# Kernel tuning notes

Measured on AMD Instinct MI355X. Metric: run time of the kernel, lower is better.

## Reference

```python
import jax, jax.numpy as jnp
import numpy as np

B, N, DIN, DOUT = 8, 2048, 256, 256

def setup_inputs() -> dict:
    key = jax.random.key(0)
    k1, k2, k3 = jax.random.split(key, 3)
    H = jax.random.normal(k1, (B, N, DIN), dtype=jnp.float32)
    G = jax.random.uniform(k2, (B, N, N), dtype=jnp.float32)  # positive -> nonzero row/col sums
    # xavier_uniform-style scale for the weight
    limit = float(np.sqrt(6.0 / (DIN + DOUT)))
    W = jax.random.uniform(k3, (DIN, DOUT), dtype=jnp.float32, minval=-limit, maxval=limit)
    return {"H": H, "G": G, "W": W}

def reference(H, G, W):
    # N_e = H @ W : [b,n,dout]
    N_e = H @ W
    # symmetric part
    G_F = (G + jnp.swapaxes(G, 1, 2)) * 0.5
    # loop over k of outer products == two normalized Gram matrices:
    # G_Sin[i,j] = sum_k G[k,i]*G[k,j] / rowsum_k  == G^T diag(1/rowsum) G
    # G_So[i,j]  = sum_k G[i,k]*G[j,k] / colsum_k  == G diag(1/colsum) G^T
    rs = G.sum(axis=-1)  # [b,n] row sums
    cs = G.sum(axis=-2)  # [b,n] col sums
    G_Sin = jnp.einsum('bki,bkj->bij', G / rs[:, :, None], G)
    G_So = jnp.einsum('bik,bjk->bij', G / cs[:, None, :], G)
    H_out = jnp.concatenate([
        jax.nn.relu(G_F @ N_e),
        jax.nn.relu(G_Sin @ N_e),
        jax.nn.relu(G_So @ N_e),
    ], axis=-1)  # [b,n,3*dout]
    return H_out
```

## Files before the change

kernel.cpp:

```cpp
#include <hip/hip_runtime.h>
#include <hip/hip_bf16.h>


constexpr int NN = 2048;
constexpr long GSTR = (long)NN * NN;
constexpr long SDN = 256L * 2048;

using frag8   = __attribute__((ext_vector_type(8))) short;
using floatx4 = __attribute__((ext_vector_type(4))) float;
using ush8    = __attribute__((ext_vector_type(8))) unsigned short;

__device__ inline unsigned short f2bf(float x) {
    unsigned u = __float_as_uint(x);
    u += 0x7FFF + ((u >> 16) & 1);
    return (unsigned short)(u >> 16);
}
__device__ inline float bf2f(unsigned short h) {
    return __uint_as_float((unsigned)h << 16);
}
__device__ inline ushort2 pk2(float a, float b) {
    union { __hip_bfloat162 h; ushort2 u; } cv;
    cv.h = __float22bfloat162_rn(float2{a, b});
    return cv.u;
}
__device__ inline void gload_lds16(const void* g, void* l) {
    __builtin_amdgcn_global_load_lds(
        (const __attribute__((address_space(1))) void*)g,
        (__attribute__((address_space(3))) void*)l, 16, 0, 0);
}

template <int PHASE>
__global__ __launch_bounds__(256) void gemmF(
    const unsigned short* __restrict__ Aa,
    const unsigned short* __restrict__ Ab,
    const unsigned short* __restrict__ Gb,
    const unsigned short* __restrict__ GbT,
    unsigned short* __restrict__ C0,
    unsigned short* __restrict__ C1,
    float* __restrict__ outp,
    const float* __restrict__ s0,
    const float* __restrict__ s1)
{
    constexpr int TM = 256, NT = 32;
    __shared__ __align__(16) unsigned short SH[2][(TM + 64) * 64];

    const int bx = blockIdx.x;
    const int bb = bx & 7;
    const int rr_ = bx >> 3;
    const int jt = rr_ & 31;
    const int h  = rr_ >> 5;
    const int j0 = jt * 64;

    const unsigned short* Ap =
        ((PHASE == 1 && h) ? Ab : Aa) + (long)bb * SDN;
    const unsigned short* Bp =
        (((PHASE == 0) == (h == 0)) ? Gb : GbT) + (long)bb * GSTR;

    const int t = threadIdx.x;
    const int w = t >> 6, l = t & 63;
    const int wm = w >> 1, wn = w & 1;
    const int quad = l >> 4, c15 = l & 15;
    const int lr = l >> 3, ls = l & 7;

    floatx4 acc[8][2] = {};

    auto stage = [&](int buf, int k0) {
        #pragma unroll
        for (int q = 0; q < 8; ++q) {
            const int rt = q * 32 + w * 8;
            gload_lds16(Ap + (long)(rt + lr) * 2048 + k0 + ((ls ^ lr) << 3),
                        &SH[buf][rt * 64]);
        }
        const unsigned short* Bt = Bp + (((long)(j0 >> 7) * 16 + (k0 >> 7)) << 14);
        const int rb = j0 & 127, kin = k0 & 127;
        #pragma unroll
        for (int q = 0; q < 2; ++q) {
            const int rt = q * 32 + w * 8;
            gload_lds16(Bt + (rb + rt + lr) * 128 + kin + ((ls ^ lr) << 3),
                        &SH[buf][TM * 64 + rt * 64]);
        }
    };

    stage(0, 0);
    asm volatile("s_waitcnt vmcnt(0)" ::: "memory");
    __builtin_amdgcn_s_barrier();
    __builtin_amdgcn_sched_barrier(0);

    int cur = 0;
    for (int tt = 0; tt < NT; ++tt) {
        if (tt + 1 < NT) stage(cur ^ 1, (tt + 1) << 6);
        __builtin_amdgcn_sched_barrier(0);
        #pragma unroll
        for (int ks = 0; ks < 2; ++ks) {
            frag8 af[8], bfv[2];
            const int swr = c15 & 7;
            #pragma unroll
            for (int mt = 0; mt < 8; ++mt)
                af[mt] = *(const frag8*)&SH[cur][(wm * 128 + mt * 16 + c15) * 64
                                                + (((ks * 4 + quad) ^ swr) << 3)];
            #pragma unroll
            for (int nt = 0; nt < 2; ++nt)
                bfv[nt] = *(const frag8*)&SH[cur][TM * 64 + (wn * 32 + nt * 16 + c15) * 64
                                                 + (((ks * 4 + quad) ^ swr) << 3)];
            #pragma unroll
            for (int mt = 0; mt < 8; ++mt)
                #pragma unroll
                for (int nt = 0; nt < 2; ++nt)
                    acc[mt][nt] = __builtin_amdgcn_mfma_f32_16x16x32_bf16(
                        af[mt], bfv[nt], acc[mt][nt], 0, 0, 0);
        }
        if (tt + 1 < NT) {
            asm volatile("s_waitcnt vmcnt(0)" ::: "memory");
            __builtin_amdgcn_s_barrier();
            __builtin_amdgcn_sched_barrier(0);
        }
        cur ^= 1;
    }

    __syncthreads();

    if constexpr (PHASE == 0) {
        unsigned short* T16 = &SH[0][0];
        #pragma unroll
        for (int nt = 0; nt < 2; ++nt) {
            const int jc = wn * 32 + nt * 16 + c15;
            const float sc = (h ? s1 : s0)[(long)bb * 2048 + j0 + jc];
            #pragma unroll
            for (int mt = 0; mt < 8; ++mt) {
                const floatx4 v = acc[mt][nt];
                const int ib = wm * 128 + mt * 16 + quad * 4;
                #pragma unroll
                for (int e = 0; e < 4; ++e)
                    T16[(ib + e) * 72 + jc] = f2bf(v[e] * sc);
            }
        }
        __syncthreads();
        unsigned short* Co = (h ? C1 : C0) + ((long)bb * 256 + t) * 2048 + j0;
        const unsigned short* Tr = T16 + t * 72;
        #pragma unroll
        for (int c2 = 0; c2 < 8; ++c2)
            *(ush8*)(Co + c2 * 8) = *(const ush8*)(Tr + c2 * 8);
    } else {
        float* TF = (float*)&SH[0][0];
        #pragma unroll
        for (int nt = 0; nt < 2; ++nt) {
            const int jc = wn * 32 + nt * 16 + c15;
            #pragma unroll
            for (int mt = 0; mt < 8; ++mt) {
                const floatx4 v = acc[mt][nt];
                const int ib = wm * 128 + mt * 16 + quad * 4;
                #pragma unroll
                for (int e = 0; e < 4; ++e)
                    TF[jc * 260 + ib + e] = fmaxf(v[e], 0.f);
            }
        }
        __syncthreads();
        const int jr = t >> 2, iq = t & 3;
        float* Op = outp + ((long)bb * 2048 + j0 + jr) * 768 + (h ? 512 : 256) + iq * 64;
        const float* Sp = TF + jr * 260 + iq * 64;
        #pragma unroll
        for (int c2 = 0; c2 < 16; ++c2)
            *(float4*)(Op + c2 * 4) = *(const float4*)(Sp + c2 * 4);
    }
}

__global__ __launch_bounds__(256) void out0k(
    const unsigned short* __restrict__ M1sT, const unsigned short* __restrict__ M2sT,
    const float* __restrict__ rs_raw, const float* __restrict__ cs_raw,
    float* __restrict__ outp)
{
    const int bb = blockIdx.y, jt = blockIdx.x;
    const int j0 = jt * 64;
    const int t = threadIdx.x;
    const int w = t >> 6, l = t & 63;
    const int rg = l >> 3, c = l & 7;
    const int ib = w * 64 + rg * 8;
    const int jb = j0 + c * 8;
    const long ab = (long)bb * SDN;

    union RowU { ush8 v; unsigned u4[4]; unsigned short a[8]; };
    RowU r1[8], r2[8], c1[8], c2[8];
    #pragma unroll
    for (int r = 0; r < 8; ++r) {
        r1[r].v = *(const ush8*)(M1sT + ab + (long)(ib + r) * 2048 + jb);
        r2[r].v = *(const ush8*)(M2sT + ab + (long)(ib + r) * 2048 + jb);
    }
    __builtin_amdgcn_sched_barrier(0);
    #pragma unroll
    for (int p = 0; p < 4; ++p)
        #pragma unroll
        for (int k = 0; k < 4; ++k) {
            const unsigned a1 = r1[2*p].u4[k], b1 = r1[2*p+1].u4[k];
            c1[2*k].u4[p]   = (a1 & 0xffffu) | (b1 << 16);
            c1[2*k+1].u4[p] = (a1 >> 16) | (b1 & 0xffff0000u);
            const unsigned a2 = r2[2*p].u4[k], b2 = r2[2*p+1].u4[k];
            c2[2*k].u4[p]   = (a2 & 0xffffu) | (b2 << 16);
            c2[2*k+1].u4[p] = (a2 >> 16) | (b2 & 0xffff0000u);
        }
    #pragma unroll
    for (int jj = 0; jj < 8; ++jj) {
        const int j = jb + jj;
        const float rr = rs_raw[(long)bb * 2048 + j];
        const float cc = cs_raw[(long)bb * 2048 + j];
        float4 o0, o1;
        o0.x = fmaxf(0.5f * (bf2f(c1[jj].a[0]) * rr + bf2f(c2[jj].a[0]) * cc), 0.f);
        o0.y = fmaxf(0.5f * (bf2f(c1[jj].a[1]) * rr + bf2f(c2[jj].a[1]) * cc), 0.f);
        o0.z = fmaxf(0.5f * (bf2f(c1[jj].a[2]) * rr + bf2f(c2[jj].a[2]) * cc), 0.f);
        o0.w = fmaxf(0.5f * (bf2f(c1[jj].a[3]) * rr + bf2f(c2[jj].a[3]) * cc), 0.f);
        o1.x = fmaxf(0.5f * (bf2f(c1[jj].a[4]) * rr + bf2f(c2[jj].a[4]) * cc), 0.f);
        o1.y = fmaxf(0.5f * (bf2f(c1[jj].a[5]) * rr + bf2f(c2[jj].a[5]) * cc), 0.f);
        o1.z = fmaxf(0.5f * (bf2f(c1[jj].a[6]) * rr + bf2f(c2[jj].a[6]) * cc), 0.f);
        o1.w = fmaxf(0.5f * (bf2f(c1[jj].a[7]) * rr + bf2f(c2[jj].a[7]) * cc), 0.f);
        float* op = outp + ((long)bb * 2048 + j) * 768 + ib;
        *(float4*)op       = o0;
        *(float4*)(op + 4) = o1;
    }
}

__global__ __launch_bounds__(256) void gemmNE(
    const unsigned short* __restrict__ Hbf,
    const unsigned short* __restrict__ Wt,
    unsigned short* __restrict__ NeT)
{
    constexpr int TM = 128, K = 256, NT = 4;
    __shared__ __align__(16) unsigned short As[2][TM * 64];
    __shared__ __align__(16) unsigned short Bs[2][64 * 64];

    const int t  = threadIdx.x;
    const int bx = blockIdx.x;
    const int xcd = bx & 7;
    const int kk  = bx >> 3;
    const int itile = xcd + 8 * (kk >> 5);
    const int rem   = kk & 31;
    const int bb    = rem >> 2;
    const int jt    = rem & 3;
    const int i0b = itile * TM;
    const int j0  = jt * 64;

    const unsigned short* Btb = Wt + (long)j0 * K;
    const unsigned short* Ab  = Hbf + (long)bb * SDN;

    const int w = t >> 6, l = t & 63;
    const int wm = w >> 1, wn = w & 1;
    const int quad = l >> 4, c15 = l & 15;
    const int lr = l >> 3, ls = l & 7;

    floatx4 acc[4][2] = {};

    auto stage = [&](int buf, int k0) {
        const unsigned short* Au = Ab + (((long)itile * 2 + (k0 >> 7)) << 14);
        const int kin = k0 & 127;
        #pragma unroll
        for (int q = 0; q < 4; ++q) {
            const int rt = q * 32 + w * 8;
            gload_lds16(Au + (rt + lr) * 128 + kin + ((ls ^ lr) << 3),
                        &As[buf][rt * 64]);
        }
        #pragma unroll
        for (int q = 0; q < 2; ++q) {
            const int rt = q * 32 + w * 8;
            gload_lds16(Btb + (long)(rt + lr) * K + k0 + ((ls ^ lr) << 3),
                        &Bs[buf][rt * 64]);
        }
    };

    stage(0, 0);
    asm volatile("s_waitcnt vmcnt(0)" ::: "memory");
    __builtin_amdgcn_s_barrier();
    __builtin_amdgcn_sched_barrier(0);

    int cur = 0;
    for (int tt = 0; tt < NT; ++tt) {
        if (tt + 1 < NT) stage(cur ^ 1, (tt + 1) << 6);
        __builtin_amdgcn_sched_barrier(0);
        #pragma unroll
        for (int ks = 0; ks < 2; ++ks) {
            frag8 af[4], bfv[2];
            const int swr = c15 & 7;
            #pragma unroll
            for (int mt = 0; mt < 4; ++mt)
                af[mt] = *(const frag8*)&As[cur][(wm * 64 + mt * 16 + c15) * 64
                                               + (((ks * 4 + quad) ^ swr) << 3)];
            #pragma unroll
            for (int nt = 0; nt < 2; ++nt)
                bfv[nt] = *(const frag8*)&Bs[cur][(wn * 32 + nt * 16 + c15) * 64
                                                + (((ks * 4 + quad) ^ swr) << 3)];
            #pragma unroll
            for (int mt = 0; mt < 4; ++mt)
                #pragma unroll
                for (int nt = 0; nt < 2; ++nt)
                    acc[mt][nt] = __builtin_amdgcn_mfma_f32_16x16x32_bf16(
                        af[mt], bfv[nt], acc[mt][nt], 0, 0, 0);
        }
        if (tt + 1 < NT) {
            asm volatile("s_waitcnt vmcnt(0)" ::: "memory");
            __builtin_amdgcn_s_barrier();
            __builtin_amdgcn_sched_barrier(0);
        }
        cur ^= 1;
    }

    #pragma unroll
    for (int mt = 0; mt < 4; ++mt) {
        const int ib = i0b + wm * 64 + mt * 16 + quad * 4;
        #pragma unroll
        for (int nt = 0; nt < 2; ++nt) {
            const floatx4 v = acc[mt][nt];
            const int gj = j0 + wn * 32 + nt * 16 + c15;
            union { ushort4 v; ushort2 u2[2]; } p;
            p.u2[0] = pk2(v[0], v[1]); p.u2[1] = pk2(v[2], v[3]);
            *(ushort4*)(NeT + ((long)bb * 256 + gj) * 2048 + ib) = p.v;
        }
    }
}

__global__ __launch_bounds__(256) void cvt_stream(
    const float* __restrict__ G,
    unsigned short* __restrict__ Gbf,
    float* __restrict__ pcs,
    float* __restrict__ inv_rs, float* __restrict__ rs_raw)
{
    __shared__ float sm[4][16];
    const int b  = blockIdx.y;
    const int s  = blockIdx.x;
    const int i0 = s * 16;
    const int t  = threadIdx.x;
    const int c8 = t * 8;
    const int w  = t >> 6, l = t & 63;

    const float* gp = G + (long)b * GSTR + (long)i0 * NN + c8;
    unsigned short* gb = Gbf + (long)b * GSTR;
    const int tc = c8 >> 7, cin = c8 & 127;

    float csum[8] = {};
    float rp[16];

    #pragma unroll
    for (int r = 0; r < 16; ++r) {
        const float4 x0 = *(const float4*)(gp + (long)r * NN);
        const float4 x1 = *(const float4*)(gp + (long)r * NN + 4);
        union { ush8 v; ushort2 u2[4]; } pk;
        pk.u2[0] = pk2(x0.x, x0.y); pk.u2[1] = pk2(x0.z, x0.w);
        pk.u2[2] = pk2(x1.x, x1.y); pk.u2[3] = pk2(x1.z, x1.w);
        const int gi = i0 + r;
        *(ush8*)(gb + (((long)(gi >> 7) * 16 + tc) << 14) + ((gi & 127) << 7) + cin) = pk.v;
        rp[r] = x0.x + x0.y + x0.z + x0.w + x1.x + x1.y + x1.z + x1.w;
        csum[0] += x0.x; csum[1] += x0.y; csum[2] += x0.z; csum[3] += x0.w;
        csum[4] += x1.x; csum[5] += x1.y; csum[6] += x1.z; csum[7] += x1.w;
    }

    float* pp = pcs + ((long)b * 128 + s) * NN + c8;
    *(float4*)pp       = make_float4(csum[0], csum[1], csum[2], csum[3]);
    *(float4*)(pp + 4) = make_float4(csum[4], csum[5], csum[6], csum[7]);

    #pragma unroll
    for (int r = 0; r < 16; ++r) {
        rp[r] += __shfl_xor(rp[r], 1);
        rp[r] += __shfl_xor(rp[r], 2);
        rp[r] += __shfl_xor(rp[r], 4);
        rp[r] += __shfl_xor(rp[r], 8);
        rp[r] += __shfl_xor(rp[r], 16);
        rp[r] += __shfl_xor(rp[r], 32);
    }
    if (l == 0) {
        #pragma unroll
        for (int r = 0; r < 16; ++r) sm[w][r] = rp[r];
    }
    __syncthreads();
    if (t < 16) {
        const float s_ = sm[0][t] + sm[1][t] + sm[2][t] + sm[3][t];
        rs_raw[(long)b * NN + i0 + t] = s_;
        inv_rs[(long)b * NN + i0 + t] = 1.0f / s_;
    }
}

__global__ __launch_bounds__(256) void cvt_t(
    const unsigned short* __restrict__ Gbf, unsigned short* __restrict__ GbfT)
{
    const int b  = blockIdx.z;
    const int tr = blockIdx.y, tc = blockIdx.x;
    const long src = (long)b * GSTR + (((long)tr * 16 + tc) << 14);
    const long dst = (long)b * GSTR + (((long)tc * 16 + tr) << 14);
    const int t = threadIdx.x;
    const int w = t >> 6, l = t & 63;
    const int wm = w >> 1, wn = w & 1;
    const int rg = l >> 3, c = l & 7;
    const int il = wm * 64 + rg * 8;
    const int jl = wn * 64 + c * 8;

    union RowU { ush8 v; unsigned u4[4]; };
    RowU rows[8], cols[8];
    #pragma unroll
    for (int r = 0; r < 8; ++r)
        rows[r].v = *(const ush8*)(Gbf + src + (long)(il + r) * 128 + jl);
    __builtin_amdgcn_sched_barrier(0);

    #pragma unroll
    for (int p = 0; p < 4; ++p)
        #pragma unroll
        for (int k = 0; k < 4; ++k) {
            const unsigned a = rows[2 * p].u4[k], bq = rows[2 * p + 1].u4[k];
            cols[2 * k].u4[p]     = (a & 0xffffu) | (bq << 16);
            cols[2 * k + 1].u4[p] = (a >> 16) | (bq & 0xffff0000u);
        }
    #pragma unroll
    for (int j = 0; j < 8; ++j)
        *(ush8*)(GbfT + dst + (long)(jl + j) * 128 + il) = cols[j].v;
}

__global__ __launch_bounds__(256) void cvt_h(
    const float* __restrict__ H, unsigned short* __restrict__ Hbf)
{
    const int b = blockIdx.y, it = blockIdx.x;
    const int t = threadIdx.x;
    const int rsub = t >> 5, c = (t & 31) * 8;
    const float* hp = H + ((long)b * 2048 + (long)it * 128) * 256;
    unsigned short* ob = Hbf + (long)b * SDN + (((long)it * 2 + (c >> 7)) << 14);
    const int cin = c & 127;
    #pragma unroll
    for (int rr = 0; rr < 16; ++rr) {
        const int r = rr * 8 + rsub;
        const float4 x0 = *(const float4*)(hp + (long)r * 256 + c);
        const float4 x1 = *(const float4*)(hp + (long)r * 256 + c + 4);
        union { ush8 v; ushort2 u2[4]; } pk;
        pk.u2[0] = pk2(x0.x, x0.y); pk.u2[1] = pk2(x0.z, x0.w);
        pk.u2[2] = pk2(x1.x, x1.y); pk.u2[3] = pk2(x1.z, x1.w);
        *(ush8*)(ob + r * 128 + cin) = pk.v;
    }
}

__global__ __launch_bounds__(256) void finalize(
    const float* __restrict__ pcs,
    float* __restrict__ inv_cs, float* __restrict__ cs_raw,
    const float* __restrict__ W, unsigned short* __restrict__ Wt)
{
    const int idx = blockIdx.x * 256 + threadIdx.x;
    if (blockIdx.y == 0) {
        const int b = idx >> 11, i = idx & 2047;
        float s = 0.f;
        for (int ic = 0; ic < 128; ++ic) s += pcs[((long)b * 128 + ic) * NN + i];
        inv_cs[idx] = 1.0f / s;
        cs_raw[idx] = s;
    } else {
        #pragma unroll
        for (int e = 0; e < 4; ++e) {
            const int flat = idx * 4 + e;
            const int j = flat >> 8, k = flat & 255;
            Wt[flat] = f2bf(W[(long)k * 256 + j]);
        }
    }
}

extern "C" void kernel_launch(void* const* d_in, const int* in_sizes, int n_in,
                              void* d_out, int out_size, void* d_ws, size_t ws_size,
                              hipStream_t stream)
{
    constexpr int B = 8;
    const float* H = (const float*)d_in[0];
    const float* G = (const float*)d_in[1];
    const float* W = (const float*)d_in[2];
    float* out = (float*)d_out;

    unsigned short* ws16 = (unsigned short*)d_ws;
    unsigned short* Gbf  = ws16;
    unsigned short* GbfT = Gbf  + (long)B * GSTR;
    unsigned short* Wt   = GbfT + (long)B * GSTR;
    unsigned short* NeT  = Wt   + 65536;
    unsigned short* M1sT = NeT  + 4194304;
    unsigned short* M2sT = M1sT + 4194304;
    unsigned short* Hbf  = M2sT + 4194304;
    float* inv_rs = (float*)(Hbf + 4194304);
    float* rs_raw = inv_rs + 16384;
    float* inv_cs = rs_raw + 16384;
    float* cs_raw = inv_cs + 16384;
    float* pcs    = cs_raw + 16384;

    cvt_stream<<<dim3(128, 8), 256, 0, stream>>>(G, Gbf, pcs, inv_rs, rs_raw);
    cvt_t<<<dim3(16, 16, 8), 256, 0, stream>>>(Gbf, GbfT);
    cvt_h<<<dim3(16, 8), 256, 0, stream>>>(H, Hbf);
    finalize<<<dim3(64, 2), 256, 0, stream>>>(pcs, inv_cs, cs_raw, W, Wt);

    gemmNE<<<512, 256, 0, stream>>>(Hbf, Wt, NeT);
    gemmF<0><<<512, 256, 0, stream>>>(NeT, nullptr, Gbf, GbfT,
                                      M1sT, M2sT, nullptr, inv_rs, inv_cs);
    gemmF<1><<<512, 256, 0, stream>>>(M1sT, M2sT, Gbf, GbfT,
                                      nullptr, nullptr, out, nullptr, nullptr);
    out0k<<<dim3(32, 8), 256, 0, stream>>>(M1sT, M2sT, rs_raw, cs_raw, out);
}
```

Baseline: 358.4 us.

## Fuse H conversion into gemmNE and out0 epilogue into gemmF phase 1

Removes the cvt_h kernel by having gemmNE read fp32 H directly and convert it to bf16 while staging into LDS, using a smaller 64-row tile and a non-double-buffered loop with more blocks. Folds the out0k kernel into the tail of gemmF<1> blocks with h==0, reusing their rs/cs pointers. Swaps the order of B and A tile loads in the gemmF stage. This saves two launches and the Hbf round-trip, but gemmNE loses its async double buffering, and the fused out0 tail reads M1sT/M2sT that other blocks of the same launch also read.

```diff
diff --git a/kernel.cpp b/kernel.cpp
--- a/kernel.cpp
+++ b/kernel.cpp
@@ -65,19 +65,19 @@
     floatx4 acc[8][2] = {};
 
     auto stage = [&](int buf, int k0) {
+        const unsigned short* Bt = Bp + (((long)(j0 >> 7) * 16 + (k0 >> 7)) << 14);
+        const int rb = j0 & 127, kin = k0 & 127;
+        #pragma unroll
+        for (int q = 0; q < 2; ++q) {
+            const int rt = q * 32 + w * 8;
+            gload_lds16(Bt + (rb + rt + lr) * 128 + kin + ((ls ^ lr) << 3),
+                        &SH[buf][TM * 64 + rt * 64]);
+        }
         #pragma unroll
         for (int q = 0; q < 8; ++q) {
             const int rt = q * 32 + w * 8;
             gload_lds16(Ap + (long)(rt + lr) * 2048 + k0 + ((ls ^ lr) << 3),
                         &SH[buf][rt * 64]);
-        }
-        const unsigned short* Bt = Bp + (((long)(j0 >> 7) * 16 + (k0 >> 7)) << 14);
-        const int rb = j0 & 127, kin = k0 & 127;
-        #pragma unroll
-        for (int q = 0; q < 2; ++q) {
-            const int rt = q * 32 + w * 8;
-            gload_lds16(Bt + (rb + rt + lr) * 128 + kin + ((ls ^ lr) << 3),
-                        &SH[buf][TM * 64 + rt * 64]);
         }
     };
 
@@ -161,70 +161,62 @@
         #pragma unroll
         for (int c2 = 0; c2 < 16; ++c2)
             *(float4*)(Op + c2 * 4) = *(const float4*)(Sp + c2 * 4);
-    }
-}
-
-__global__ __launch_bounds__(256) void out0k(
-    const unsigned short* __restrict__ M1sT, const unsigned short* __restrict__ M2sT,
-    const float* __restrict__ rs_raw, const float* __restrict__ cs_raw,
-    float* __restrict__ outp)
-{
-    const int bb = blockIdx.y, jt = blockIdx.x;
-    const int j0 = jt * 64;
-    const int t = threadIdx.x;
-    const int w = t >> 6, l = t & 63;
-    const int rg = l >> 3, c = l & 7;
-    const int ib = w * 64 + rg * 8;
-    const int jb = j0 + c * 8;
-    const long ab = (long)bb * SDN;
-
-    union RowU { ush8 v; unsigned u4[4]; unsigned short a[8]; };
-    RowU r1[8], r2[8], c1[8], c2[8];
-    #pragma unroll
-    for (int r = 0; r < 8; ++r) {
-        r1[r].v = *(const ush8*)(M1sT + ab + (long)(ib + r) * 2048 + jb);
-        r2[r].v = *(const ush8*)(M2sT + ab + (long)(ib + r) * 2048 + jb);
-    }
-    __builtin_amdgcn_sched_barrier(0);
-    #pragma unroll
-    for (int p = 0; p < 4; ++p)
-        #pragma unroll
-        for (int k = 0; k < 4; ++k) {
-            const unsigned a1 = r1[2*p].u4[k], b1 = r1[2*p+1].u4[k];
-            c1[2*k].u4[p]   = (a1 & 0xffffu) | (b1 << 16);
-            c1[2*k+1].u4[p] = (a1 >> 16) | (b1 & 0xffff0000u);
-            const unsigned a2 = r2[2*p].u4[k], b2 = r2[2*p+1].u4[k];
-            c2[2*k].u4[p]   = (a2 & 0xffffu) | (b2 << 16);
-            c2[2*k+1].u4[p] = (a2 >> 16) | (b2 & 0xffff0000u);
-        }
-    #pragma unroll
-    for (int jj = 0; jj < 8; ++jj) {
-        const int j = jb + jj;
-        const float rr = rs_raw[(long)bb * 2048 + j];
-        const float cc = cs_raw[(long)bb * 2048 + j];
-        float4 o0, o1;
-        o0.x = fmaxf(0.5f * (bf2f(c1[jj].a[0]) * rr + bf2f(c2[jj].a[0]) * cc), 0.f);
-        o0.y = fmaxf(0.5f * (bf2f(c1[jj].a[1]) * rr + bf2f(c2[jj].a[1]) * cc), 0.f);
-        o0.z = fmaxf(0.5f * (bf2f(c1[jj].a[2]) * rr + bf2f(c2[jj].a[2]) * cc), 0.f);
-        o0.w = fmaxf(0.5f * (bf2f(c1[jj].a[3]) * rr + bf2f(c2[jj].a[3]) * cc), 0.f);
-        o1.x = fmaxf(0.5f * (bf2f(c1[jj].a[4]) * rr + bf2f(c2[jj].a[4]) * cc), 0.f);
-        o1.y = fmaxf(0.5f * (bf2f(c1[jj].a[5]) * rr + bf2f(c2[jj].a[5]) * cc), 0.f);
-        o1.z = fmaxf(0.5f * (bf2f(c1[jj].a[6]) * rr + bf2f(c2[jj].a[6]) * cc), 0.f);
-        o1.w = fmaxf(0.5f * (bf2f(c1[jj].a[7]) * rr + bf2f(c2[jj].a[7]) * cc), 0.f);
-        float* op = outp + ((long)bb * 2048 + j) * 768 + ib;
-        *(float4*)op       = o0;
-        *(float4*)(op + 4) = o1;
+
+        if (h == 0) {
+            const int w0 = t >> 6, l0 = t & 63;
+            const int rg0 = l0 >> 3, c0 = l0 & 7;
+            const int ib0 = w0 * 64 + rg0 * 8;
+            const int jb0 = j0 + c0 * 8;
+            const long ab = (long)bb * SDN;
+
+            union RowU { ush8 v; unsigned u4[4]; unsigned short a[8]; };
+            RowU r1[8], r2[8], c1[8], c2v[8];
+            #pragma unroll
+            for (int r = 0; r < 8; ++r) {
+                r1[r].v = *(const ush8*)(Aa + ab + (long)(ib0 + r) * 2048 + jb0);
+                r2[r].v = *(const ush8*)(Ab + ab + (long)(ib0 + r) * 2048 + jb0);
+            }
+            #pragma unroll
+            for (int p = 0; p < 4; ++p)
+                #pragma unroll
+                for (int k = 0; k < 4; ++k) {
+                    const unsigned a1 = r1[2*p].u4[k], b1 = r1[2*p+1].u4[k];
+                    c1[2*k].u4[p]   = (a1 & 0xffffu) | (b1 << 16);
+                    c1[2*k+1].u4[p] = (a1 >> 16) | (b1 & 0xffff0000u);
+                    const unsigned a2 = r2[2*p].u4[k], b2 = r2[2*p+1].u4[k];
+                    c2v[2*k].u4[p]   = (a2 & 0xffffu) | (b2 << 16);
+                    c2v[2*k+1].u4[p] = (a2 >> 16) | (b2 & 0xffff0000u);
+                }
+            #pragma unroll
+            for (int jj = 0; jj < 8; ++jj) {
+                const int j = jb0 + jj;
+                const float rr = s0[(long)bb * 2048 + j];
+                const float cc = s1[(long)bb * 2048 + j];
+                float4 o0, o1;
+                o0.x = fmaxf(0.5f * (bf2f(c1[jj].a[0]) * rr + bf2f(c2v[jj].a[0]) * cc), 0.f);
+                o0.y = fmaxf(0.5f * (bf2f(c1[jj].a[1]) * rr + bf2f(c2v[jj].a[1]) * cc), 0.f);
+                o0.z = fmaxf(0.5f * (bf2f(c1[jj].a[2]) * rr + bf2f(c2v[jj].a[2]) * cc), 0.f);
+                o0.w = fmaxf(0.5f * (bf2f(c1[jj].a[3]) * rr + bf2f(c2v[jj].a[3]) * cc), 0.f);
+                o1.x = fmaxf(0.5f * (bf2f(c1[jj].a[4]) * rr + bf2f(c2v[jj].a[4]) * cc), 0.f);
+                o1.y = fmaxf(0.5f * (bf2f(c1[jj].a[5]) * rr + bf2f(c2v[jj].a[5]) * cc), 0.f);
+                o1.z = fmaxf(0.5f * (bf2f(c1[jj].a[6]) * rr + bf2f(c2v[jj].a[6]) * cc), 0.f);
+                o1.w = fmaxf(0.5f * (bf2f(c1[jj].a[7]) * rr + bf2f(c2v[jj].a[7]) * cc), 0.f);
+                float* op = outp + ((long)bb * 2048 + j) * 768 + ib0;
+                *(float4*)op       = o0;
+                *(float4*)(op + 4) = o1;
+            }
+        }
     }
 }
 
 __global__ __launch_bounds__(256) void gemmNE(
-    const unsigned short* __restrict__ Hbf,
+    const float* __restrict__ H,
     const unsigned short* __restrict__ Wt,
     unsigned short* __restrict__ NeT)
 {
-    constexpr int TM = 128, K = 256, NT = 4;
-    __shared__ __align__(16) unsigned short As[2][TM * 64];
-    __shared__ __align__(16) unsigned short Bs[2][64 * 64];
+    constexpr int TM = 64, K = 256;
+    __shared__ __align__(16) unsigned short As[TM * 64];
+    __shared__ __align__(16) unsigned short Bs[64 * 64];
 
     const int t  = threadIdx.x;
     const int bx = blockIdx.x;
@@ -238,71 +230,64 @@
     const int j0  = jt * 64;
 
     const unsigned short* Btb = Wt + (long)j0 * K;
-    const unsigned short* Ab  = Hbf + (long)bb * SDN;
+    const float* Af = H + (long)bb * (2048L * 256);
 
     const int w = t >> 6, l = t & 63;
     const int wm = w >> 1, wn = w & 1;
     const int quad = l >> 4, c15 = l & 15;
     const int lr = l >> 3, ls = l & 7;
 
-    floatx4 acc[4][2] = {};
-
-    auto stage = [&](int buf, int k0) {
-        const unsigned short* Au = Ab + (((long)itile * 2 + (k0 >> 7)) << 14);
-        const int kin = k0 & 127;
-        #pragma unroll
-        for (int q = 0; q < 4; ++q) {
-            const int rt = q * 32 + w * 8;
-            gload_lds16(Au + (rt + lr) * 128 + kin + ((ls ^ lr) << 3),
-                        &As[buf][rt * 64]);
-        }
+    floatx4 acc[2][2] = {};
+
+    for (int k0 = 0; k0 < K; k0 += 64) {
+        const int ar  = t >> 2;
+        const int ac0 = (t & 3) * 2;
+        const float* ap = Af + (long)(i0b + ar) * 256 + k0 + ac0 * 8;
+        const float4 x0 = *(const float4*)(ap + 0);
+        const float4 x1 = *(const float4*)(ap + 4);
+        const float4 x2 = *(const float4*)(ap + 8);
+        const float4 x3 = *(const float4*)(ap + 12);
+        union { ush8 v; ushort2 u2[4]; } p0, p1;
+        p0.u2[0] = pk2(x0.x, x0.y); p0.u2[1] = pk2(x0.z, x0.w);
+        p0.u2[2] = pk2(x1.x, x1.y); p0.u2[3] = pk2(x1.z, x1.w);
+        p1.u2[0] = pk2(x2.x, x2.y); p1.u2[1] = pk2(x2.z, x2.w);
+        p1.u2[2] = pk2(x3.x, x3.y); p1.u2[3] = pk2(x3.z, x3.w);
+        const int sw = ar & 7;
+        *(ush8*)&As[ar * 64 + ((ac0 ^ sw) << 3)]       = p0.v;
+        *(ush8*)&As[ar * 64 + (((ac0 + 1) ^ sw) << 3)] = p1.v;
         #pragma unroll
         for (int q = 0; q < 2; ++q) {
-            const int rt = q * 32 + w * 8;
+            const int rt = w * 16 + q * 8;
             gload_lds16(Btb + (long)(rt + lr) * K + k0 + ((ls ^ lr) << 3),
-                        &Bs[buf][rt * 64]);
-        }
-    };
-
-    stage(0, 0);
-    asm volatile("s_waitcnt vmcnt(0)" ::: "memory");
-    __builtin_amdgcn_s_barrier();
-    __builtin_amdgcn_sched_barrier(0);
-
-    int cur = 0;
-    for (int tt = 0; tt < NT; ++tt) {
-        if (tt + 1 < NT) stage(cur ^ 1, (tt + 1) << 6);
-        __builtin_amdgcn_sched_barrier(0);
+                        &Bs[rt * 64]);
+        }
+        __syncthreads();
+
         #pragma unroll
         for (int ks = 0; ks < 2; ++ks) {
-            frag8 af[4], bfv[2];
+            frag8 af[2], bfv[2];
             const int swr = c15 & 7;
             #pragma unroll
-            for (int mt = 0; mt < 4; ++mt)
-                af[mt] = *(const frag8*)&As[cur][(wm * 64 + mt * 16 + c15) * 64
-                                               + (((ks * 4 + quad) ^ swr) << 3)];
+            for (int mt = 0; mt < 2; ++mt)
+                af[mt] = *(const frag8*)&As[(wm * 32 + mt * 16 + c15) * 64
+                                            + (((ks * 4 + quad) ^ swr) << 3)];
             #pragma unroll
             for (int nt = 0; nt < 2; ++nt)
-                bfv[nt] = *(const frag8*)&Bs[cur][(wn * 32 + nt * 16 + c15) * 64
-                                                + (((ks * 4 + quad) ^ swr) << 3)];
-            #pragma unroll
-            for (int mt = 0; mt < 4; ++mt)
+                bfv[nt] = *(const frag8*)&Bs[(wn * 32 + nt * 16 + c15) * 64
+                                             + (((ks * 4 + quad) ^ swr) << 3)];
+            #pragma unroll
+            for (int mt = 0; mt < 2; ++mt)
                 #pragma unroll
                 for (int nt = 0; nt < 2; ++nt)
                     acc[mt][nt] = __builtin_amdgcn_mfma_f32_16x16x32_bf16(
                         af[mt], bfv[nt], acc[mt][nt], 0, 0, 0);
         }
-        if (tt + 1 < NT) {
-            asm volatile("s_waitcnt vmcnt(0)" ::: "memory");
-            __builtin_amdgcn_s_barrier();
-            __builtin_amdgcn_sched_barrier(0);
-        }
-        cur ^= 1;
-    }
-
-    #pragma unroll
-    for (int mt = 0; mt < 4; ++mt) {
-        const int ib = i0b + wm * 64 + mt * 16 + quad * 4;
+        __syncthreads();
+    }
+
+    #pragma unroll
+    for (int mt = 0; mt < 2; ++mt) {
+        const int ib = i0b + wm * 32 + mt * 16 + quad * 4;
         #pragma unroll
         for (int nt = 0; nt < 2; ++nt) {
             const floatx4 v = acc[mt][nt];
@@ -408,27 +393,6 @@
         *(ush8*)(GbfT + dst + (long)(jl + j) * 128 + il) = cols[j].v;
 }
 
-__global__ __launch_bounds__(256) void cvt_h(
-    const float* __restrict__ H, unsigned short* __restrict__ Hbf)
-{
-    const int b = blockIdx.y, it = blockIdx.x;
-    const int t = threadIdx.x;
-    const int rsub = t >> 5, c = (t & 31) * 8;
-    const float* hp = H + ((long)b * 2048 + (long)it * 128) * 256;
-    unsigned short* ob = Hbf + (long)b * SDN + (((long)it * 2 + (c >> 7)) << 14);
-    const int cin = c & 127;
-    #pragma unroll
-    for (int rr = 0; rr < 16; ++rr) {
-        const int r = rr * 8 + rsub;
-        const float4 x0 = *(const float4*)(hp + (long)r * 256 + c);
-        const float4 x1 = *(const float4*)(hp + (long)r * 256 + c + 4);
-        union { ush8 v; ushort2 u2[4]; } pk;
-        pk.u2[0] = pk2(x0.x, x0.y); pk.u2[1] = pk2(x0.z, x0.w);
-        pk.u2[2] = pk2(x1.x, x1.y); pk.u2[3] = pk2(x1.z, x1.w);
-        *(ush8*)(ob + r * 128 + cin) = pk.v;
-    }
-}
-
 __global__ __launch_bounds__(256) void finalize(
     const float* __restrict__ pcs,
     float* __restrict__ inv_cs, float* __restrict__ cs_raw,
@@ -468,8 +432,7 @@
     unsigned short* NeT  = Wt   + 65536;
     unsigned short* M1sT = NeT  + 4194304;
     unsigned short* M2sT = M1sT + 4194304;
-    unsigned short* Hbf  = M2sT + 4194304;
-    float* inv_rs = (float*)(Hbf + 4194304);
+    float* inv_rs = (float*)(M2sT + 4194304);
     float* rs_raw = inv_rs + 16384;
     float* inv_cs = rs_raw + 16384;
     float* cs_raw = inv_cs + 16384;
@@ -477,13 +440,11 @@
 
     cvt_stream<<<dim3(128, 8), 256, 0, stream>>>(G, Gbf, pcs, inv_rs, rs_raw);
     cvt_t<<<dim3(16, 16, 8), 256, 0, stream>>>(Gbf, GbfT);
-    cvt_h<<<dim3(16, 8), 256, 0, stream>>>(H, Hbf);
     finalize<<<dim3(64, 2), 256, 0, stream>>>(pcs, inv_cs, cs_raw, W, Wt);
 
-    gemmNE<<<512, 256, 0, stream>>>(Hbf, Wt, NeT);
+    gemmNE<<<1024, 256, 0, stream>>>(H, Wt, NeT);
     gemmF<0><<<512, 256, 0, stream>>>(NeT, nullptr, Gbf, GbfT,
                                       M1sT, M2sT, nullptr, inv_rs, inv_cs);
     gemmF<1><<<512, 256, 0, stream>>>(M1sT, M2sT, Gbf, GbfT,
-                                      nullptr, nullptr, out, nullptr, nullptr);
-    out0k<<<dim3(32, 8), 256, 0, stream>>>(M1sT, M2sT, rs_raw, cs_raw, out);
-}
+                                      nullptr, nullptr, out, rs_raw, cs_raw);
+}
```

New measurement: 359.2 us. No clear change (+0.2%).
